# Kernel optimization log

Hardware: AMD Instinct MI355X
Metric: run time of the kernel (lower is better)

The kernel has to match this reference:

```python
import jax, jax.numpy as jnp
import numpy as np

ALPHA = 1.1
COMMISSION = 0.05
BET_PCT = 0.02
B = 4_194_304
T = 6  # num traps


def setup_inputs() -> dict:
    key = jax.random.key(0)
    k1, k2, k3, k4 = jax.random.split(key, 4)
    predicted_probs = jax.random.uniform(k1, (B, T), dtype=jnp.float32)
    true_winners = (jax.random.uniform(k2, (B, T)) > 0.8).astype(jnp.float32)
    market_odds = jax.random.uniform(k3, (B, T), dtype=jnp.float32) * 10.0
    invalid = jax.random.uniform(k4, (B, 1)) < 0.1
    market_odds = jnp.where(invalid, 0.0, market_odds)
    return {"predicted_probs": predicted_probs, "true_winners": true_winners,
            "market_odds": market_odds}


def reference(predicted_probs, true_winners, market_odds):
    batch_size = predicted_probs.shape[0]
    payout_scale = BET_PCT * (1.0 - COMMISSION)

    has_valid_odds = jnp.any(market_odds > 0, axis=1)  # [B]
    # expected profit per dog; zero for races without valid odds
    ep = (market_odds * ALPHA * predicted_probs - 1.0) * payout_scale  # [B,T]
    ep = jnp.where(has_valid_odds[:, None], ep, 0.0)

    best_idx = jnp.argmax(ep, axis=1)  # [B], first-max like torch
    best_ep = jnp.take_along_axis(ep, best_idx[:, None], axis=1)[:, 0]  # [B]
    should_bet = (best_ep > 0) & has_valid_odds  # [B]

    # actual profits (not part of the differentiable loss; tracked as metrics)
    odds_b = jnp.take_along_axis(market_odds, best_idx[:, None], axis=1)[:, 0]
    win_b = jnp.take_along_axis(true_winners, best_idx[:, None], axis=1)[:, 0]
    win_profit = (odds_b * ALPHA * BET_PCT - BET_PCT) * (1.0 - COMMISSION)
    lose_profit = -BET_PCT * (1.0 - COMMISSION)
    actual_profits = jnp.where(should_bet,
                               jnp.where(win_b > 0.5, win_profit, lose_profit),
                               0.0)

    any_bet = jnp.any(should_bet)
    sum_bet_ep = jnp.sum(jnp.where(should_bet, best_ep, 0.0))
    fallback = -jnp.mean(jnp.max(predicted_probs, axis=1)) * 0.1
    total_expected_profit = jnp.where(any_bet, sum_bet_ep, fallback)
    loss = -total_expected_profit / batch_size

    batch_profit = jnp.sum(actual_profits)
    num_bets = jnp.sum(should_bet.astype(jnp.int32))
    return loss, batch_profit, num_bets
```

## Files before the change

kernel.cpp:

```cpp
#include <hip/hip_runtime.h>
#include <math.h>


constexpr int T = 6;
constexpr int NBLK = 2048;
constexpr int NTHR = 256;

__global__ __launch_bounds__(NTHR) void betting_stage1(
    const float4* __restrict__ probs,
    const float4* __restrict__ winners,
    const float4* __restrict__ odds,
    double* __restrict__ partials,
    int npairs)
{
    const float ALPHA = 1.1f;
    const float BET = 0.02f;
    const float KEEP = 0.95f;
    const float PS = BET * KEEP;

    double s_ep = 0.0, s_profit = 0.0, s_maxp = 0.0;
    int cnt = 0;

    const int stride = gridDim.x * blockDim.x;
    for (int i = blockIdx.x * blockDim.x + threadIdx.x; i < npairs; i += stride) {
        const size_t base = (size_t)i * 3;
        float4 pa = probs[base + 0], pb = probs[base + 1], pc = probs[base + 2];
        float4 oa = odds [base + 0], ob = odds [base + 1], oc = odds [base + 2];
        float4 wa = winners[base + 0], wb = winners[base + 1], wc = winners[base + 2];

        float p[12] = {pa.x, pa.y, pa.z, pa.w, pb.x, pb.y, pb.z, pb.w, pc.x, pc.y, pc.z, pc.w};
        float o[12] = {oa.x, oa.y, oa.z, oa.w, ob.x, ob.y, ob.z, ob.w, oc.x, oc.y, oc.z, oc.w};
        float w[12] = {wa.x, wa.y, wa.z, wa.w, wb.x, wb.y, wb.z, wb.w, wc.x, wc.y, wc.z, wc.w};

        #pragma unroll
        for (int rr = 0; rr < 2; ++rr) {
            const int off = rr * T;
            bool valid = false;
            float maxp = p[off];
            float best_ep = -INFINITY;
            float best_odds = 0.0f, best_win = 0.0f;
            #pragma unroll
            for (int j = 0; j < T; ++j) {
                const float oj = o[off + j];
                const float pj = p[off + j];
                valid |= (oj > 0.0f);
                maxp = fmaxf(maxp, pj);
                const float ep = (oj * ALPHA * pj - 1.0f) * PS;
                if (ep > best_ep) {
                    best_ep = ep;
                    best_odds = oj;
                    best_win = w[off + j];
                }
            }
            s_maxp += (double)maxp;

            const bool bet = valid && (best_ep > 0.0f);
            s_ep += bet ? (double)best_ep : 0.0;
            cnt += bet ? 1 : 0;
            const float profit = (best_win > 0.5f)
                ? (best_odds * ALPHA * BET - BET) * KEEP
                : -BET * KEEP;
            s_profit += bet ? (double)profit : 0.0;
        }
    }

    #pragma unroll
    for (int off = 32; off > 0; off >>= 1) {
        s_ep     += __shfl_down(s_ep, off);
        s_profit += __shfl_down(s_profit, off);
        s_maxp   += __shfl_down(s_maxp, off);
        cnt      += __shfl_down(cnt, off);
    }

    __shared__ double sm_ep[NTHR / 64];
    __shared__ double sm_pr[NTHR / 64];
    __shared__ double sm_mx[NTHR / 64];
    __shared__ int    sm_ct[NTHR / 64];
    const int lane = threadIdx.x & 63;
    const int wid  = threadIdx.x >> 6;
    if (lane == 0) {
        sm_ep[wid] = s_ep; sm_pr[wid] = s_profit; sm_mx[wid] = s_maxp; sm_ct[wid] = cnt;
    }
    __syncthreads();
    if (threadIdx.x == 0) {
        double t_ep = 0.0, t_pr = 0.0, t_mx = 0.0; int t_ct = 0;
        #pragma unroll
        for (int i = 0; i < NTHR / 64; ++i) {
            t_ep += sm_ep[i]; t_pr += sm_pr[i]; t_mx += sm_mx[i]; t_ct += sm_ct[i];
        }
        double* slot = partials + (size_t)blockIdx.x * 4;
        slot[0] = t_ep; slot[1] = t_pr; slot[2] = t_mx; slot[3] = (double)t_ct;
    }
}

__global__ __launch_bounds__(NTHR) void betting_stage2(
    const double* __restrict__ partials, float* __restrict__ out, int nblk, int B)
{
    double s_ep = 0.0, s_pr = 0.0, s_mx = 0.0, s_ct = 0.0;
    for (int i = threadIdx.x; i < nblk; i += blockDim.x) {
        const double* slot = partials + (size_t)i * 4;
        s_ep += slot[0]; s_pr += slot[1]; s_mx += slot[2]; s_ct += slot[3];
    }
    #pragma unroll
    for (int off = 32; off > 0; off >>= 1) {
        s_ep += __shfl_down(s_ep, off);
        s_pr += __shfl_down(s_pr, off);
        s_mx += __shfl_down(s_mx, off);
        s_ct += __shfl_down(s_ct, off);
    }
    __shared__ double sm[4][NTHR / 64];
    const int lane = threadIdx.x & 63;
    const int wid  = threadIdx.x >> 6;
    if (lane == 0) { sm[0][wid] = s_ep; sm[1][wid] = s_pr; sm[2][wid] = s_mx; sm[3][wid] = s_ct; }
    __syncthreads();
    if (threadIdx.x == 0) {
        double ep = 0.0, pr = 0.0, mx = 0.0, ct = 0.0;
        #pragma unroll
        for (int i = 0; i < NTHR / 64; ++i) { ep += sm[0][i]; pr += sm[1][i]; mx += sm[2][i]; ct += sm[3][i]; }
        bool any_bet = ct > 0.0;
        double total = any_bet ? ep : (-(mx / (double)B) * 0.1);
        out[0] = (float)(-total / (double)B);
        out[1] = (float)pr;
        out[2] = (float)ct;
    }
}

extern "C" void kernel_launch(void* const* d_in, const int* in_sizes, int n_in,
                              void* d_out, int out_size, void* d_ws, size_t ws_size,
                              hipStream_t stream) {
    const float* probs   = (const float*)d_in[0];
    const float* winners = (const float*)d_in[1];
    const float* odds    = (const float*)d_in[2];
    float* out = (float*)d_out;
    const int B = in_sizes[0] / T;
    const int npairs = B / 2;

    double* partials = (double*)d_ws;

    betting_stage1<<<NBLK, NTHR, 0, stream>>>(
        (const float4*)probs, (const float4*)winners, (const float4*)odds, partials, npairs);
    betting_stage2<<<1, NTHR, 0, stream>>>(partials, out, NBLK, B);
}
```

Measured before the change: 281.5 us.

## Stage inputs through LDS with global_load_lds for coalesced chunked access

Replaces the strided per-thread float4 loads, where each thread read 3 consecutive float4s per array, with block-wide coalesced async copies straight into LDS using global_load_lds. Threads then read their 12 floats from LDS and load only the single winner value at the argmax index. The goal is better coalescing and less register pressure on this bandwidth-bound reduction. The grid also shrinks to 1024 blocks, and each chunk now needs two barriers and 36KB of LDS, which may cost occupancy.

```diff
diff --git a/kernel.cpp b/kernel.cpp
--- a/kernel.cpp
+++ b/kernel.cpp
@@ -3,16 +3,31 @@
 
 
 constexpr int T = 6;
-constexpr int NBLK = 2048;
 constexpr int NTHR = 256;
+constexpr int NBLK = 1024;
+constexpr int CHUNK_PAIRS = 256;
+constexpr int F4_PER_ARR = CHUNK_PAIRS * 3;
+
+typedef float f4 __attribute__((ext_vector_type(4)));
+
+__device__ __forceinline__ void stage16(const f4* g, f4* l) {
+    __builtin_amdgcn_global_load_lds(
+        (const __attribute__((address_space(1))) void*)g,
+        (__attribute__((address_space(3))) void*)l,
+        16, 0, 0);
+}
 
 __global__ __launch_bounds__(NTHR) void betting_stage1(
-    const float4* __restrict__ probs,
-    const float4* __restrict__ winners,
-    const float4* __restrict__ odds,
+    const f4* __restrict__ probs4,
+    const f4* __restrict__ winners4,
+    const f4* __restrict__ odds4,
     double* __restrict__ partials,
     int npairs)
 {
+    __shared__ f4 lp[F4_PER_ARR];
+    __shared__ f4 lo[F4_PER_ARR];
+    __shared__ f4 lw[F4_PER_ARR];
+
     const float ALPHA = 1.1f;
     const float BET = 0.02f;
     const float KEEP = 0.95f;
@@ -21,17 +36,67 @@
     double s_ep = 0.0, s_profit = 0.0, s_maxp = 0.0;
     int cnt = 0;
 
-    const int stride = gridDim.x * blockDim.x;
-    for (int i = blockIdx.x * blockDim.x + threadIdx.x; i < npairs; i += stride) {
-        const size_t base = (size_t)i * 3;
-        float4 pa = probs[base + 0], pb = probs[base + 1], pc = probs[base + 2];
-        float4 oa = odds [base + 0], ob = odds [base + 1], oc = odds [base + 2];
-        float4 wa = winners[base + 0], wb = winners[base + 1], wc = winners[base + 2];
-
-        float p[12] = {pa.x, pa.y, pa.z, pa.w, pb.x, pb.y, pb.z, pb.w, pc.x, pc.y, pc.z, pc.w};
-        float o[12] = {oa.x, oa.y, oa.z, oa.w, ob.x, ob.y, ob.z, ob.w, oc.x, oc.y, oc.z, oc.w};
-        float w[12] = {wa.x, wa.y, wa.z, wa.w, wb.x, wb.y, wb.z, wb.w, wc.x, wc.y, wc.z, wc.w};
-
+    const int t = threadIdx.x;
+    const int nchunks = npairs / CHUNK_PAIRS;
+
+    for (int c = blockIdx.x; c < nchunks; c += gridDim.x) {
+        const size_t gb = (size_t)c * F4_PER_ARR;
+        #pragma unroll
+        for (int k = 0; k < 3; ++k) {
+            const int idx = k * NTHR + t;
+            stage16(probs4   + gb + idx, &lp[idx]);
+            stage16(odds4    + gb + idx, &lo[idx]);
+            stage16(winners4 + gb + idx, &lw[idx]);
+        }
+        __syncthreads();
+
+        const float* rp = (const float*)lp + t * 12;
+        const float* ro = (const float*)lo + t * 12;
+        const float* rw = (const float*)lw + t * 12;
+        f4 P0 = *(const f4*)(rp);  f4 P1 = *(const f4*)(rp + 4);  f4 P2 = *(const f4*)(rp + 8);
+        f4 O0 = *(const f4*)(ro);  f4 O1 = *(const f4*)(ro + 4);  f4 O2 = *(const f4*)(ro + 8);
+        float p[12] = {P0.x, P0.y, P0.z, P0.w, P1.x, P1.y, P1.z, P1.w, P2.x, P2.y, P2.z, P2.w};
+        float o[12] = {O0.x, O0.y, O0.z, O0.w, O1.x, O1.y, O1.z, O1.w, O2.x, O2.y, O2.z, O2.w};
+
+        #pragma unroll
+        for (int rr = 0; rr < 2; ++rr) {
+            const int off = rr * T;
+            bool valid = false;
+            float maxp = p[off];
+            float best_ep = -INFINITY;
+            float best_odds = 0.0f;
+            int bestj = 0;
+            #pragma unroll
+            for (int j = 0; j < T; ++j) {
+                const float oj = o[off + j];
+                const float pj = p[off + j];
+                valid |= (oj > 0.0f);
+                maxp = fmaxf(maxp, pj);
+                const float ep = (oj * ALPHA * pj - 1.0f) * PS;
+                if (ep > best_ep) { best_ep = ep; best_odds = oj; bestj = j; }
+            }
+            s_maxp += (double)maxp;
+            const bool bet = valid && (best_ep > 0.0f);
+            const float wbest = rw[off + bestj];
+            s_ep += bet ? (double)best_ep : 0.0;
+            cnt += bet ? 1 : 0;
+            const float profit = (wbest > 0.5f)
+                ? (best_odds * ALPHA * BET - BET) * KEEP
+                : -BET * KEEP;
+            s_profit += bet ? (double)profit : 0.0;
+        }
+        __syncthreads();
+    }
+
+    for (int i = nchunks * CHUNK_PAIRS + blockIdx.x * NTHR + t;
+         i < npairs; i += gridDim.x * NTHR) {
+        const size_t b = (size_t)i * 3;
+        f4 P0 = probs4[b], P1 = probs4[b + 1], P2 = probs4[b + 2];
+        f4 O0 = odds4[b],  O1 = odds4[b + 1],  O2 = odds4[b + 2];
+        f4 W0 = winners4[b], W1 = winners4[b + 1], W2 = winners4[b + 2];
+        float p[12] = {P0.x, P0.y, P0.z, P0.w, P1.x, P1.y, P1.z, P1.w, P2.x, P2.y, P2.z, P2.w};
+        float o[12] = {O0.x, O0.y, O0.z, O0.w, O1.x, O1.y, O1.z, O1.w, O2.x, O2.y, O2.z, O2.w};
+        float w[12] = {W0.x, W0.y, W0.z, W0.w, W1.x, W1.y, W1.z, W1.w, W2.x, W2.y, W2.z, W2.w};
         #pragma unroll
         for (int rr = 0; rr < 2; ++rr) {
             const int off = rr * T;
@@ -46,14 +111,9 @@
                 valid |= (oj > 0.0f);
                 maxp = fmaxf(maxp, pj);
                 const float ep = (oj * ALPHA * pj - 1.0f) * PS;
-                if (ep > best_ep) {
-                    best_ep = ep;
-                    best_odds = oj;
-                    best_win = w[off + j];
-                }
+                if (ep > best_ep) { best_ep = ep; best_odds = oj; best_win = w[off + j]; }
             }
             s_maxp += (double)maxp;
-
             const bool bet = valid && (best_ep > 0.0f);
             s_ep += bet ? (double)best_ep : 0.0;
             cnt += bet ? 1 : 0;
@@ -76,17 +136,17 @@
     __shared__ double sm_pr[NTHR / 64];
     __shared__ double sm_mx[NTHR / 64];
     __shared__ int    sm_ct[NTHR / 64];
-    const int lane = threadIdx.x & 63;
-    const int wid  = threadIdx.x >> 6;
+    const int lane = t & 63;
+    const int wid  = t >> 6;
     if (lane == 0) {
         sm_ep[wid] = s_ep; sm_pr[wid] = s_profit; sm_mx[wid] = s_maxp; sm_ct[wid] = cnt;
     }
     __syncthreads();
-    if (threadIdx.x == 0) {
+    if (t == 0) {
         double t_ep = 0.0, t_pr = 0.0, t_mx = 0.0; int t_ct = 0;
         #pragma unroll
-        for (int i = 0; i < NTHR / 64; ++i) {
-            t_ep += sm_ep[i]; t_pr += sm_pr[i]; t_mx += sm_mx[i]; t_ct += sm_ct[i];
+        for (int k = 0; k < NTHR / 64; ++k) {
+            t_ep += sm_ep[k]; t_pr += sm_pr[k]; t_mx += sm_mx[k]; t_ct += sm_ct[k];
         }
         double* slot = partials + (size_t)blockIdx.x * 4;
         slot[0] = t_ep; slot[1] = t_pr; slot[2] = t_mx; slot[3] = (double)t_ct;
@@ -116,7 +176,7 @@
     if (threadIdx.x == 0) {
         double ep = 0.0, pr = 0.0, mx = 0.0, ct = 0.0;
         #pragma unroll
-        for (int i = 0; i < NTHR / 64; ++i) { ep += sm[0][i]; pr += sm[1][i]; mx += sm[2][i]; ct += sm[3][i]; }
+        for (int k = 0; k < NTHR / 64; ++k) { ep += sm[0][k]; pr += sm[1][k]; mx += sm[2][k]; ct += sm[3][k]; }
         bool any_bet = ct > 0.0;
         double total = any_bet ? ep : (-(mx / (double)B) * 0.1);
         out[0] = (float)(-total / (double)B);
@@ -138,6 +198,6 @@
     double* partials = (double*)d_ws;
 
     betting_stage1<<<NBLK, NTHR, 0, stream>>>(
-        (const float4*)probs, (const float4*)winners, (const float4*)odds, partials, npairs);
+        (const f4*)probs, (const f4*)winners, (const f4*)odds, partials, npairs);
     betting_stage2<<<1, NTHR, 0, stream>>>(partials, out, NBLK, B);
 }
```

Measured after the change: 281.2 us. No clear change (-0.1%).
